# Optimization experiments

Measured on AMD Instinct MI355X. Metric: run time of the kernel, lower is better.

Reference implementation:

```python
import jax, jax.numpy as jnp
import numpy as np

N, M, H, D_IN, D_OUT = 131072, 256, 1024, 512, 512


def setup_inputs() -> dict:
    key = jax.random.key(0)
    ks = jax.random.split(key, 26)
    s = 0.05  # small init scale so gates/softplus stay in a sane range
    rn = lambda k, sh, sc=1.0: jax.random.normal(k, sh, jnp.float32) * sc
    ru = lambda k, sh: jax.random.uniform(k, sh, dtype=jnp.float32)
    pw = ru(ks[5], (2, 1, N))
    pw = pw / jnp.sum(pw, axis=-1, keepdims=True)  # prev weights are attention distributions
    return {
        'x': rn(ks[0], (1, D_IN)),
        'prev_read': rn(ks[1], (1, M)),
        'h_state': rn(ks[2], (1, H), s),
        'c_state': rn(ks[3], (1, H), s),
        'memory': ru(ks[4], (1, N, M)),
        'prev_w': pw,
        'W_ih': rn(ks[6], (4 * H, D_IN + M), s),
        'b_ih': rn(ks[7], (4 * H,), s),
        'W_hh': rn(ks[8], (4 * H, H), s),
        'b_hh': rn(ks[9], (4 * H,), s),
        'W_out': rn(ks[10], (D_OUT, H + M), s),
        'b_out': rn(ks[11], (D_OUT,), s),
        'Wk': rn(ks[12], (2, M, H), s),
        'bk': rn(ks[13], (2, M), s),
        'Wbeta': rn(ks[14], (2, H), s),
        'bbeta': rn(ks[15], (2,), s),
        'Wg': rn(ks[16], (2, H), s),
        'bg': rn(ks[17], (2,), s),
        'Ws': rn(ks[18], (2, 3, H), s),
        'bs': rn(ks[19], (2, 3), s),
        'Wgamma': rn(ks[20], (2, H), s),
        'bgamma': rn(ks[21], (2,), s),
        'We': rn(ks[22], (2, M, H), s),
        'be': rn(ks[23], (2, M), s),
        'Wa': rn(ks[24], (2, M, H), s),
        'ba': rn(ks[25], (2, M), s),
    }


def _ntm_step(x, prev_read, h_state, c_state, memory, prev_w, W_ih, b_ih, W_hh,
              b_hh, W_out, b_out, Wk, bk, Wbeta, bbeta, Wg, bg, Ws, bs,
              Wgamma, bgamma, We, be, Wa, ba):
    # ---- LSTMCell controller (torch gate order: i, f, g, o) ----
    lstm_in = jnp.concatenate([x, prev_read], axis=1)  # [1, D_IN+M]
    gates = lstm_in @ W_ih.T + b_ih + h_state @ W_hh.T + b_hh
    i_g, f_g, g_g, o_g = jnp.split(gates, 4, axis=1)
    c = jax.nn.sigmoid(f_g) * c_state + jax.nn.sigmoid(i_g) * jnp.tanh(g_g)
    h = jax.nn.sigmoid(o_g) * jnp.tanh(c)

    EPS_COS, EPS_SHARP = 1e-8, 1e-16

    def head_addr(idx, mem):
        # heads are driven by the CELL state (as in the original code)
        key_v = jnp.tanh(c @ Wk[idx].T + bk[idx])                              # [1, M]
        beta = jax.nn.softplus(jnp.sum(c * Wbeta[idx], 1, keepdims=True) + bbeta[idx])
        gate = jax.nn.sigmoid(jnp.sum(c * Wg[idx], 1, keepdims=True) + bg[idx])
        shift = jax.nn.softmax(c @ Ws[idx].T + bs[idx], axis=1)                # [1, 3]
        gamma = 1.0 + jax.nn.softplus(jnp.sum(c * Wgamma[idx], 1, keepdims=True) + bgamma[idx])
        # content addressing: cosine similarity against all N rows
        dots = jnp.einsum('bm,bnm->bn', key_v, mem)                            # [1, N]
        kn = jnp.maximum(jnp.linalg.norm(key_v, axis=1, keepdims=True), EPS_COS)
        mn = jnp.maximum(jnp.linalg.norm(mem, axis=2), EPS_COS)
        cw = jax.nn.softmax(beta * dots / (kn * mn), axis=1)
        # gated interpolation with previous weights
        gw = gate * cw + (1.0 - gate) * prev_w[idx]
        # 3-tap circular convolution shift (== conv1d on circularly padded w)
        sw = (shift[:, 0:1] * jnp.roll(gw, 1, axis=1)
              + shift[:, 1:2] * gw
              + shift[:, 2:3] * jnp.roll(gw, -1, axis=1))
        wp = sw ** gamma  # sharpening
        return wp / (jnp.sum(wp, 1, keepdims=True) + EPS_SHARP)

    # head 0: read (operates on pre-write memory)
    w_r = head_addr(0, memory)
    read = jnp.einsum('bn,bnm->bm', w_r, memory)                               # [1, M]
    # head 1: write (erase then add)
    w_w = head_addr(1, memory)
    erase = jax.nn.sigmoid(c @ We[1].T + be[1])                                # [1, M]
    add = jnp.tanh(c @ Wa[1].T + ba[1])                                        # [1, M]
    new_mem = memory * (1.0 - w_w[:, :, None] * erase[:, None, :]) \
              + w_w[:, :, None] * add[:, None, :]
    # external output
    out = jax.nn.sigmoid(jnp.concatenate([h, read], axis=1) @ W_out.T + b_out)
    return out, new_mem


def reference(x, prev_read, h_state, c_state, memory, prev_w, W_ih, b_ih, W_hh,
              b_hh, W_out, b_out, Wk, bk, Wbeta, bbeta, Wg, bg, Ws, bs,
              Wgamma, bgamma, We, be, Wa, ba):
    return _ntm_step(x, prev_read, h_state, c_state, memory, prev_w, W_ih, b_ih,
                     W_hh, b_hh, W_out, b_out, Wk, bk, Wbeta, bbeta, Wg, bg,
                     Ws, bs, Wgamma, bgamma, We, be, Wa, ba)
```

## Files before the change

### kernel.cpp

```cpp
#include <hip/hip_runtime.h>
#include <math.h>

#define NN 131072
#define MM 256
#define HH 1024

#define WS_P      0
#define WS_GATES  64
#define WS_KEY    4160
#define WS_ER     4672
#define WS_AD     4928
#define WS_E      8192
#define WS_WP     270336
#define WS_PSUM   532480
#define WS_PSUM2  548864
#define WS_RPART  549888
#define WS_READ   812032

#define P_RAWB   0
#define P_RAWG   2
#define P_RAWGA  4
#define P_RAWS   6
#define P_SSCALE 12
#define P_GATE   14
#define P_GAMMA  16
#define P_SHIFT  18
#define P_INVS   26
#define P_WSCALE 28

__device__ __forceinline__ float wave_sum(float v) {
    v += __shfl_xor(v, 32); v += __shfl_xor(v, 16); v += __shfl_xor(v, 8);
    v += __shfl_xor(v, 4);  v += __shfl_xor(v, 2);  v += __shfl_xor(v, 1);
    return v;
}
__device__ __forceinline__ float sigm(float x) { return 1.0f / (1.0f + expf(-x)); }
__device__ __forceinline__ float softplus_(float x) { return x > 20.0f ? x : log1pf(expf(x)); }
__device__ __forceinline__ float dot4(float4 a, float4 b) {
    return a.x * b.x + a.y * b.y + a.z * b.z + a.w * b.w;
}

__global__ __launch_bounds__(256) void gates_kernel(
    const float* __restrict__ x, const float* __restrict__ pr, const float* __restrict__ hs,
    const float* __restrict__ Wih, const float* __restrict__ bih,
    const float* __restrict__ Whh, const float* __restrict__ bhh,
    float* __restrict__ gates)
{
    int wid = blockIdx.x * 4 + (threadIdx.x >> 6);
    int lane = threadIdx.x & 63;
    const float4* wi4 = (const float4*)(Wih + (size_t)wid * 768);
    const float4* wh4 = (const float4*)(Whh + (size_t)wid * 1024);
    const float4* x4  = (const float4*)x;
    const float4* pr4 = (const float4*)pr;
    const float4* hs4 = (const float4*)hs;
    float s = 0.f;
    #pragma unroll
    for (int q = 0; q < 3; q++) {
        int j4 = lane + 64 * q;
        float4 wv = wi4[j4];
        float4 xv = (q < 2) ? x4[j4] : pr4[j4 - 128];
        s += dot4(wv, xv);
    }
    #pragma unroll
    for (int q = 0; q < 4; q++) {
        int j4 = lane + 64 * q;
        s += dot4(wh4[j4], hs4[j4]);
    }
    s = wave_sum(s);
    if (lane == 0) gates[wid] = s + bih[wid] + bhh[wid];
}

__global__ __launch_bounds__(256) void head_prep_kernel(
    const float* __restrict__ gates, const float* __restrict__ cs,
    const float* __restrict__ Wk, const float* __restrict__ bk,
    const float* __restrict__ We, const float* __restrict__ be,
    const float* __restrict__ Wa, const float* __restrict__ ba,
    const float* __restrict__ Ws, const float* __restrict__ bs,
    const float* __restrict__ Wbeta, const float* __restrict__ bbeta,
    const float* __restrict__ Wg, const float* __restrict__ bg,
    const float* __restrict__ Wgamma, const float* __restrict__ bgamma,
    float* __restrict__ key, float* __restrict__ er, float* __restrict__ ad,
    float* __restrict__ params)
{
    __shared__ float c_l[1024];
    int t = threadIdx.x;
    #pragma unroll
    for (int k = 0; k < 4; k++) {
        int j = t + 256 * k;
        float ig = gates[j], fg = gates[1024 + j], gg = gates[2048 + j];
        c_l[j] = sigm(fg) * cs[j] + sigm(ig) * tanhf(gg);
    }
    __syncthreads();

    int wid = blockIdx.x * 4 + (t >> 6);
    int lane = t & 63;
    const float* wrow; float bias; float* dst; int act;
    if (wid < 512)      { int h = wid >> 8, m = wid & 255; wrow = Wk + (size_t)(h * 256 + m) * 1024; bias = bk[h * 256 + m]; dst = key + wid; act = 0; }
    else if (wid < 768) { int m = wid - 512; wrow = We + (size_t)(256 + m) * 1024; bias = be[256 + m]; dst = er + m; act = 1; }
    else if (wid < 1024){ int m = wid - 768; wrow = Wa + (size_t)(256 + m) * 1024; bias = ba[256 + m]; dst = ad + m; act = 0; }
    else if (wid < 1030){ int k = wid - 1024; wrow = Ws + (size_t)k * 1024; bias = bs[k]; dst = params + P_RAWS + k; act = 2; }
    else                { int k = wid - 1030; int h = k & 1, which = k >> 1;
                          const float* Wp = which == 0 ? Wbeta : (which == 1 ? Wg : Wgamma);
                          const float* bp = which == 0 ? bbeta : (which == 1 ? bg : bgamma);
                          wrow = Wp + h * 1024; bias = bp[h]; dst = params + 2 * which + h; act = 2; }
    const float4* w4 = (const float4*)wrow;
    const float4* c4 = (const float4*)c_l;
    float s = 0.f;
    #pragma unroll
    for (int q = 0; q < 4; q++) {
        int j4 = lane + 64 * q;
        s += dot4(w4[j4], c4[j4]);
    }
    s = wave_sum(s);
    if (lane == 0) {
        s += bias;
        if (act == 0) s = tanhf(s);
        else if (act == 1) s = sigm(s);
        *dst = s;
    }
}

__global__ void finalize_params_kernel(const float* __restrict__ key, float* __restrict__ params)
{
    int h = threadIdx.x >> 6, lane = threadIdx.x & 63;
    float s = 0.f;
    for (int m = lane; m < 256; m += 64) { float v = key[h * 256 + m]; s += v * v; }
    s = wave_sum(s);
    if (lane == 0) {
        float kn = fmaxf(sqrtf(s), 1e-8f);
        params[P_SSCALE + h] = softplus_(params[P_RAWB + h]) / kn;
        params[P_GATE + h]   = sigm(params[P_RAWG + h]);
        params[P_GAMMA + h]  = 1.0f + softplus_(params[P_RAWGA + h]);
        float s0 = params[P_RAWS + h * 3], s1 = params[P_RAWS + h * 3 + 1], s2 = params[P_RAWS + h * 3 + 2];
        float mx = fmaxf(s0, fmaxf(s1, s2));
        float e0 = expf(s0 - mx), e1 = expf(s1 - mx), e2 = expf(s2 - mx);
        float inv = 1.0f / (e0 + e1 + e2);
        params[P_SHIFT + h * 3]     = e0 * inv;
        params[P_SHIFT + h * 3 + 1] = e1 * inv;
        params[P_SHIFT + h * 3 + 2] = e2 * inv;
    }
}

__global__ __launch_bounds__(256) void score_exp_kernel(
    const float* __restrict__ mem, const float* __restrict__ key,
    const float* __restrict__ params, float* __restrict__ e, float* __restrict__ psum)
{
    int w = threadIdx.x >> 6, lane = threadIdx.x & 63;
    int sub = lane & 15, g = lane >> 4;
    int wid = blockIdx.x * 4 + w;
    int row = wid * 4 + g;
    const float4* m4 = (const float4*)mem;
    const float4* k4 = (const float4*)key;
    float4 k0[4], k1[4], mv[4];
    #pragma unroll
    for (int q = 0; q < 4; q++) {
        k0[q] = k4[sub + 16 * q];
        k1[q] = k4[64 + sub + 16 * q];
        mv[q] = m4[(size_t)row * 64 + sub + 16 * q];
    }
    float d0 = 0.f, d1 = 0.f, sq = 0.f;
    #pragma unroll
    for (int q = 0; q < 4; q++) {
        d0 += dot4(k0[q], mv[q]);
        d1 += dot4(k1[q], mv[q]);
        sq += dot4(mv[q], mv[q]);
    }
    #pragma unroll
    for (int off = 8; off; off >>= 1) {
        d0 += __shfl_xor(d0, off); d1 += __shfl_xor(d1, off); sq += __shfl_xor(sq, off);
    }
    float a0 = 0.f, a1 = 0.f;
    if (sub == 0) {
        float mn = fmaxf(sqrtf(sq), 1e-8f);
        float s0 = params[P_SSCALE] * d0 / mn;
        float s1 = params[P_SSCALE + 1] * d1 / mn;
        a0 = expf(fminf(s0, 60.f));
        a1 = expf(fminf(s1, 60.f));
        e[row] = a0;
        e[NN + row] = a1;
    }
    a0 = wave_sum(a0); a1 = wave_sum(a1);
    __shared__ float l[8];
    if (lane == 0) { l[w] = a0; l[4 + w] = a1; }
    __syncthreads();
    if (threadIdx.x == 0) {
        psum[blockIdx.x]        = l[0] + l[1] + l[2] + l[3];
        psum[8192 + blockIdx.x] = l[4] + l[5] + l[6] + l[7];
    }
}

__global__ void reduce_inv_kernel(const float* __restrict__ psum, float* __restrict__ dst,
                                  int n, float eps)
{
    float v0 = 0.f, v1 = 0.f;
    for (int i = threadIdx.x; i < n; i += 1024) { v0 += psum[i]; v1 += psum[n + i]; }
    v0 = wave_sum(v0); v1 = wave_sum(v1);
    __shared__ float l[32];
    int w = threadIdx.x >> 6, lane = threadIdx.x & 63;
    if (lane == 0) { l[w] = v0; l[16 + w] = v1; }
    __syncthreads();
    if (threadIdx.x == 0) {
        float S0 = 0.f, S1 = 0.f;
        for (int i = 0; i < 16; i++) { S0 += l[i]; S1 += l[16 + i]; }
        dst[0] = 1.0f / (S0 + eps);
        dst[1] = 1.0f / (S1 + eps);
    }
}

__global__ __launch_bounds__(256) void shift_pow_kernel(
    const float* __restrict__ e, const float* __restrict__ pw,
    const float* __restrict__ params, float* __restrict__ wp, float* __restrict__ psum2)
{
    int tid = blockIdx.x * 256 + threadIdx.x;
    float gate0 = params[P_GATE], gate1 = params[P_GATE + 1];
    float inv0 = params[P_INVS], inv1 = params[P_INVS + 1];
    float ga0 = params[P_GAMMA], ga1 = params[P_GAMMA + 1];
    float sh00 = params[P_SHIFT], sh01 = params[P_SHIFT + 1], sh02 = params[P_SHIFT + 2];
    float sh10 = params[P_SHIFT + 3], sh11 = params[P_SHIFT + 4], sh12 = params[P_SHIFT + 5];
    float a0 = 0.f, a1 = 0.f;
    for (int h = 0; h < 2; h++) {
        int n = tid;
        int base = h << 17;
        float gate = h ? gate1 : gate0, inv = h ? inv1 : inv0, gamma = h ? ga1 : ga0;
        float s0 = h ? sh10 : sh00, s1 = h ? sh11 : sh01, s2 = h ? sh12 : sh02;
        int nm = (n - 1) & (NN - 1), np = (n + 1) & (NN - 1);
        float gwm = gate * e[base + nm] * inv + (1.f - gate) * pw[base + nm];
        float gw0 = gate * e[base + n] * inv + (1.f - gate) * pw[base + n];
        float gwp = gate * e[base + np] * inv + (1.f - gate) * pw[base + np];
        float sw = s0 * gwm + s1 * gw0 + s2 * gwp;
        float v = powf(sw, gamma);
        wp[base + n] = v;
        if (h) a1 += v; else a0 += v;
    }
    a0 = wave_sum(a0); a1 = wave_sum(a1);
    __shared__ float l[8];
    int w = threadIdx.x >> 6, lane = threadIdx.x & 63;
    if (lane == 0) { l[w] = a0; l[4 + w] = a1; }
    __syncthreads();
    if (threadIdx.x == 0) {
        psum2[blockIdx.x]       = l[0] + l[1] + l[2] + l[3];
        psum2[512 + blockIdx.x] = l[4] + l[5] + l[6] + l[7];
    }
}

__global__ __launch_bounds__(256) void update_kernel(
    const float* __restrict__ mem, const float* __restrict__ wp,
    const float* __restrict__ params, const float* __restrict__ er, const float* __restrict__ ad,
    float* __restrict__ newmem, float* __restrict__ rpart)
{
    int w = threadIdx.x >> 6, lane = threadIdx.x & 63;
    int wid = blockIdx.x * 4 + w;
    float sc0 = params[P_WSCALE], sc1 = params[P_WSCALE + 1];
    float4 e4 = ((const float4*)er)[lane];
    float4 a4 = ((const float4*)ad)[lane];
    float4 acc = make_float4(0.f, 0.f, 0.f, 0.f);
    const float4* m4 = (const float4*)mem;
    float4* o4 = (float4*)newmem;
    for (int r = 0; r < 32; r++) {
        int row = wid * 32 + r;
        float wr = wp[row] * sc0;
        float ww = wp[NN + row] * sc1;
        float4 mv = m4[(size_t)row * 64 + lane];
        float4 nm;
        nm.x = mv.x * (1.f - ww * e4.x) + ww * a4.x;
        nm.y = mv.y * (1.f - ww * e4.y) + ww * a4.y;
        nm.z = mv.z * (1.f - ww * e4.z) + ww * a4.z;
        nm.w = mv.w * (1.f - ww * e4.w) + ww * a4.w;
        o4[(size_t)row * 64 + lane] = nm;
        acc.x += wr * mv.x; acc.y += wr * mv.y; acc.z += wr * mv.z; acc.w += wr * mv.w;
    }
    __shared__ float lds[4][256];
    lds[w][lane * 4 + 0] = acc.x;
    lds[w][lane * 4 + 1] = acc.y;
    lds[w][lane * 4 + 2] = acc.z;
    lds[w][lane * 4 + 3] = acc.w;
    __syncthreads();
    int tid = threadIdx.x;
    float s = lds[0][tid] + lds[1][tid] + lds[2][tid] + lds[3][tid];
    rpart[(size_t)blockIdx.x * 256 + tid] = s;
}

__global__ __launch_bounds__(256) void read_reduce_kernel(
    const float* __restrict__ rpart, float* __restrict__ readv)
{
    int m = blockIdx.x;
    int t = threadIdx.x;
    float s = 0.f;
    #pragma unroll
    for (int k = 0; k < 4; k++) s += rpart[(size_t)(t + 256 * k) * 256 + m];
    s = wave_sum(s);
    __shared__ float l[4];
    int w = t >> 6, lane = t & 63;
    if (lane == 0) l[w] = s;
    __syncthreads();
    if (t == 0) readv[m] = l[0] + l[1] + l[2] + l[3];
}

__global__ __launch_bounds__(256) void out_kernel(
    const float* __restrict__ gates, const float* __restrict__ cs,
    const float* __restrict__ readv,
    const float* __restrict__ Wout, const float* __restrict__ bout, float* __restrict__ out)
{
    __shared__ float hl[1280];
    int t = threadIdx.x;
    #pragma unroll
    for (int k = 0; k < 4; k++) {
        int j = t + 256 * k;
        float ig = gates[j], fg = gates[1024 + j], gg = gates[2048 + j], og = gates[3072 + j];
        float cv = sigm(fg) * cs[j] + sigm(ig) * tanhf(gg);
        hl[j] = sigm(og) * tanhf(cv);
    }
    hl[1024 + t] = readv[t];
    __syncthreads();

    int wid = blockIdx.x * 4 + (t >> 6);
    int lane = t & 63;
    const float4* w4 = (const float4*)(Wout + (size_t)wid * 1280);
    const float4* h4 = (const float4*)hl;
    float s = 0.f;
    #pragma unroll
    for (int q = 0; q < 5; q++) {
        int j4 = lane + 64 * q;
        s += dot4(w4[j4], h4[j4]);
    }
    s = wave_sum(s);
    if (lane == 0) out[wid] = sigm(s + bout[wid]);
}

extern "C" void kernel_launch(void* const* d_in, const int* in_sizes, int n_in,
                              void* d_out, int out_size, void* d_ws, size_t ws_size,
                              hipStream_t stream)
{
    const float* x       = (const float*)d_in[0];
    const float* pr      = (const float*)d_in[1];
    const float* hs      = (const float*)d_in[2];
    const float* cs      = (const float*)d_in[3];
    const float* mem     = (const float*)d_in[4];
    const float* pw      = (const float*)d_in[5];
    const float* Wih     = (const float*)d_in[6];
    const float* bih     = (const float*)d_in[7];
    const float* Whh     = (const float*)d_in[8];
    const float* bhh     = (const float*)d_in[9];
    const float* Wout    = (const float*)d_in[10];
    const float* bout    = (const float*)d_in[11];
    const float* Wk      = (const float*)d_in[12];
    const float* bk      = (const float*)d_in[13];
    const float* Wbeta   = (const float*)d_in[14];
    const float* bbeta   = (const float*)d_in[15];
    const float* Wg      = (const float*)d_in[16];
    const float* bg      = (const float*)d_in[17];
    const float* Ws      = (const float*)d_in[18];
    const float* bs      = (const float*)d_in[19];
    const float* Wgamma  = (const float*)d_in[20];
    const float* bgamma  = (const float*)d_in[21];
    const float* We      = (const float*)d_in[22];
    const float* be      = (const float*)d_in[23];
    const float* Wa      = (const float*)d_in[24];
    const float* ba      = (const float*)d_in[25];

    float* ws = (float*)d_ws;
    float* P      = ws + WS_P;
    float* gates  = ws + WS_GATES;
    float* key    = ws + WS_KEY;
    float* er     = ws + WS_ER;
    float* ad     = ws + WS_AD;
    float* e      = ws + WS_E;
    float* wp     = ws + WS_WP;
    float* psum   = ws + WS_PSUM;
    float* psum2  = ws + WS_PSUM2;
    float* rpart  = ws + WS_RPART;
    float* readv  = ws + WS_READ;

    float* out    = (float*)d_out;
    float* newmem = (float*)d_out + 512;

    gates_kernel<<<1024, 256, 0, stream>>>(x, pr, hs, Wih, bih, Whh, bhh, gates);
    head_prep_kernel<<<259, 256, 0, stream>>>(gates, cs, Wk, bk, We, be, Wa, ba, Ws, bs,
                                              Wbeta, bbeta, Wg, bg, Wgamma, bgamma,
                                              key, er, ad, P);
    finalize_params_kernel<<<1, 128, 0, stream>>>(key, P);
    score_exp_kernel<<<8192, 256, 0, stream>>>(mem, key, P, e, psum);
    reduce_inv_kernel<<<1, 1024, 0, stream>>>(psum, P + P_INVS, 8192, 0.0f);
    shift_pow_kernel<<<512, 256, 0, stream>>>(e, pw, P, wp, psum2);
    reduce_inv_kernel<<<1, 1024, 0, stream>>>(psum2, P + P_WSCALE, 512, 1e-16f);
    update_kernel<<<1024, 256, 0, stream>>>(mem, wp, P, er, ad, newmem, rpart);
    read_reduce_kernel<<<256, 256, 0, stream>>>(rpart, readv);
    out_kernel<<<128, 256, 0, stream>>>(gates, cs, readv, Wout, bout, out);
}
```

Before: 109.3 us.

## Fold scalar param and reduction kernels into consumer kernel prologues

Removes the finalize_params kernel and both single-block reduce_inv launches. Each consumer block now recomputes the key norm, the 8192-entry partial-sum reduction or the 512-entry reduction redundantly in its own prologue. This cuts three serialized launches and their gaps, at the cost of redundant per-block reads and extra barriers. It also switches exp and pow to the fast intrinsics and makes the new-memory writes nontemporal stores.

```diff
diff --git a/kernel.cpp b/kernel.cpp
--- a/kernel.cpp
+++ b/kernel.cpp
@@ -4,6 +4,8 @@
 #define NN 131072
 #define MM 256
 #define HH 1024
+
+typedef float nat_f4 __attribute__((ext_vector_type(4)));
 
 #define WS_P      0
 #define WS_GATES  64
@@ -21,12 +23,6 @@
 #define P_RAWG   2
 #define P_RAWGA  4
 #define P_RAWS   6
-#define P_SSCALE 12
-#define P_GATE   14
-#define P_GAMMA  16
-#define P_SHIFT  18
-#define P_INVS   26
-#define P_WSCALE 28
 
 __device__ __forceinline__ float wave_sum(float v) {
     v += __shfl_xor(v, 32); v += __shfl_xor(v, 16); v += __shfl_xor(v, 8);
@@ -119,32 +115,28 @@
     }
 }
 
-__global__ void finalize_params_kernel(const float* __restrict__ key, float* __restrict__ params)
-{
-    int h = threadIdx.x >> 6, lane = threadIdx.x & 63;
-    float s = 0.f;
-    for (int m = lane; m < 256; m += 64) { float v = key[h * 256 + m]; s += v * v; }
-    s = wave_sum(s);
-    if (lane == 0) {
-        float kn = fmaxf(sqrtf(s), 1e-8f);
-        params[P_SSCALE + h] = softplus_(params[P_RAWB + h]) / kn;
-        params[P_GATE + h]   = sigm(params[P_RAWG + h]);
-        params[P_GAMMA + h]  = 1.0f + softplus_(params[P_RAWGA + h]);
-        float s0 = params[P_RAWS + h * 3], s1 = params[P_RAWS + h * 3 + 1], s2 = params[P_RAWS + h * 3 + 2];
-        float mx = fmaxf(s0, fmaxf(s1, s2));
-        float e0 = expf(s0 - mx), e1 = expf(s1 - mx), e2 = expf(s2 - mx);
-        float inv = 1.0f / (e0 + e1 + e2);
-        params[P_SHIFT + h * 3]     = e0 * inv;
-        params[P_SHIFT + h * 3 + 1] = e1 * inv;
-        params[P_SHIFT + h * 3 + 2] = e2 * inv;
-    }
-}
-
 __global__ __launch_bounds__(256) void score_exp_kernel(
     const float* __restrict__ mem, const float* __restrict__ key,
     const float* __restrict__ params, float* __restrict__ e, float* __restrict__ psum)
 {
-    int w = threadIdx.x >> 6, lane = threadIdx.x & 63;
+    __shared__ float ss_l[2];
+    __shared__ float red[8];
+    int t = threadIdx.x;
+    int w = t >> 6, lane = t & 63;
+    {
+        float v0 = key[t], v1 = key[256 + t];
+        float s0 = v0 * v0, s1 = v1 * v1;
+        s0 = wave_sum(s0); s1 = wave_sum(s1);
+        if (lane == 0) { red[w] = s0; red[4 + w] = s1; }
+        __syncthreads();
+        if (t == 0) {
+            float k0 = red[0] + red[1] + red[2] + red[3];
+            float k1 = red[4] + red[5] + red[6] + red[7];
+            ss_l[0] = softplus_(params[P_RAWB])     / fmaxf(sqrtf(k0), 1e-8f);
+            ss_l[1] = softplus_(params[P_RAWB + 1]) / fmaxf(sqrtf(k1), 1e-8f);
+        }
+        __syncthreads();
+    }
     int sub = lane & 15, g = lane >> 4;
     int wid = blockIdx.x * 4 + w;
     int row = wid * 4 + g;
@@ -171,52 +163,69 @@
     float a0 = 0.f, a1 = 0.f;
     if (sub == 0) {
         float mn = fmaxf(sqrtf(sq), 1e-8f);
-        float s0 = params[P_SSCALE] * d0 / mn;
-        float s1 = params[P_SSCALE + 1] * d1 / mn;
-        a0 = expf(fminf(s0, 60.f));
-        a1 = expf(fminf(s1, 60.f));
+        float s0 = ss_l[0] * d0 / mn;
+        float s1 = ss_l[1] * d1 / mn;
+        a0 = __expf(fminf(s0, 60.f));
+        a1 = __expf(fminf(s1, 60.f));
         e[row] = a0;
         e[NN + row] = a1;
     }
     a0 = wave_sum(a0); a1 = wave_sum(a1);
-    __shared__ float l[8];
-    if (lane == 0) { l[w] = a0; l[4 + w] = a1; }
-    __syncthreads();
-    if (threadIdx.x == 0) {
-        psum[blockIdx.x]        = l[0] + l[1] + l[2] + l[3];
-        psum[8192 + blockIdx.x] = l[4] + l[5] + l[6] + l[7];
-    }
-}
-
-__global__ void reduce_inv_kernel(const float* __restrict__ psum, float* __restrict__ dst,
-                                  int n, float eps)
-{
-    float v0 = 0.f, v1 = 0.f;
-    for (int i = threadIdx.x; i < n; i += 1024) { v0 += psum[i]; v1 += psum[n + i]; }
-    v0 = wave_sum(v0); v1 = wave_sum(v1);
-    __shared__ float l[32];
-    int w = threadIdx.x >> 6, lane = threadIdx.x & 63;
-    if (lane == 0) { l[w] = v0; l[16 + w] = v1; }
-    __syncthreads();
-    if (threadIdx.x == 0) {
-        float S0 = 0.f, S1 = 0.f;
-        for (int i = 0; i < 16; i++) { S0 += l[i]; S1 += l[16 + i]; }
-        dst[0] = 1.0f / (S0 + eps);
-        dst[1] = 1.0f / (S1 + eps);
+    __syncthreads();
+    if (lane == 0) { red[w] = a0; red[4 + w] = a1; }
+    __syncthreads();
+    if (t == 0) {
+        psum[blockIdx.x]        = red[0] + red[1] + red[2] + red[3];
+        psum[8192 + blockIdx.x] = red[4] + red[5] + red[6] + red[7];
     }
 }
 
 __global__ __launch_bounds__(256) void shift_pow_kernel(
     const float* __restrict__ e, const float* __restrict__ pw,
-    const float* __restrict__ params, float* __restrict__ wp, float* __restrict__ psum2)
-{
-    int tid = blockIdx.x * 256 + threadIdx.x;
-    float gate0 = params[P_GATE], gate1 = params[P_GATE + 1];
-    float inv0 = params[P_INVS], inv1 = params[P_INVS + 1];
-    float ga0 = params[P_GAMMA], ga1 = params[P_GAMMA + 1];
-    float sh00 = params[P_SHIFT], sh01 = params[P_SHIFT + 1], sh02 = params[P_SHIFT + 2];
-    float sh10 = params[P_SHIFT + 3], sh11 = params[P_SHIFT + 4], sh12 = params[P_SHIFT + 5];
+    const float* __restrict__ params, const float* __restrict__ psum,
+    float* __restrict__ wp, float* __restrict__ psum2)
+{
+    __shared__ float par[6];
+    __shared__ float shs[6];
+    __shared__ float red[8];
+    int t = threadIdx.x;
+    int w = t >> 6, lane = t & 63;
+    {
+        float v0 = 0.f, v1 = 0.f;
+        for (int i = t; i < 8192; i += 256) { v0 += psum[i]; v1 += psum[8192 + i]; }
+        v0 = wave_sum(v0); v1 = wave_sum(v1);
+        if (lane == 0) { red[w] = v0; red[4 + w] = v1; }
+        __syncthreads();
+        if (t == 0) {
+            par[0] = 1.0f / (red[0] + red[1] + red[2] + red[3]);
+            par[1] = 1.0f / (red[4] + red[5] + red[6] + red[7]);
+            par[2] = sigm(params[P_RAWG]);
+            par[3] = sigm(params[P_RAWG + 1]);
+            par[4] = 1.0f + softplus_(params[P_RAWGA]);
+            par[5] = 1.0f + softplus_(params[P_RAWGA + 1]);
+        }
+        if (t == 64) {
+            #pragma unroll
+            for (int h = 0; h < 2; h++) {
+                float s0 = params[P_RAWS + h * 3], s1 = params[P_RAWS + h * 3 + 1], s2 = params[P_RAWS + h * 3 + 2];
+                float mx = fmaxf(s0, fmaxf(s1, s2));
+                float e0 = expf(s0 - mx), e1 = expf(s1 - mx), e2 = expf(s2 - mx);
+                float inv = 1.0f / (e0 + e1 + e2);
+                shs[h * 3 + 0] = e0 * inv;
+                shs[h * 3 + 1] = e1 * inv;
+                shs[h * 3 + 2] = e2 * inv;
+            }
+        }
+        __syncthreads();
+    }
+    float gate0 = par[2], gate1 = par[3];
+    float inv0 = par[0], inv1 = par[1];
+    float ga0 = par[4], ga1 = par[5];
+    float sh00 = shs[0], sh01 = shs[1], sh02 = shs[2];
+    float sh10 = shs[3], sh11 = shs[4], sh12 = shs[5];
+    int tid = blockIdx.x * 256 + t;
     float a0 = 0.f, a1 = 0.f;
+    #pragma unroll
     for (int h = 0; h < 2; h++) {
         int n = tid;
         int base = h << 17;
@@ -227,45 +236,59 @@
         float gw0 = gate * e[base + n] * inv + (1.f - gate) * pw[base + n];
         float gwp = gate * e[base + np] * inv + (1.f - gate) * pw[base + np];
         float sw = s0 * gwm + s1 * gw0 + s2 * gwp;
-        float v = powf(sw, gamma);
+        float v = __powf(sw, gamma);
         wp[base + n] = v;
         if (h) a1 += v; else a0 += v;
     }
     a0 = wave_sum(a0); a1 = wave_sum(a1);
-    __shared__ float l[8];
-    int w = threadIdx.x >> 6, lane = threadIdx.x & 63;
-    if (lane == 0) { l[w] = a0; l[4 + w] = a1; }
-    __syncthreads();
-    if (threadIdx.x == 0) {
-        psum2[blockIdx.x]       = l[0] + l[1] + l[2] + l[3];
-        psum2[512 + blockIdx.x] = l[4] + l[5] + l[6] + l[7];
+    __syncthreads();
+    if (lane == 0) { red[w] = a0; red[4 + w] = a1; }
+    __syncthreads();
+    if (t == 0) {
+        psum2[blockIdx.x]       = red[0] + red[1] + red[2] + red[3];
+        psum2[512 + blockIdx.x] = red[4] + red[5] + red[6] + red[7];
     }
 }
 
 __global__ __launch_bounds__(256) void update_kernel(
     const float* __restrict__ mem, const float* __restrict__ wp,
-    const float* __restrict__ params, const float* __restrict__ er, const float* __restrict__ ad,
+    const float* __restrict__ psum2, const float* __restrict__ er, const float* __restrict__ ad,
     float* __restrict__ newmem, float* __restrict__ rpart)
 {
-    int w = threadIdx.x >> 6, lane = threadIdx.x & 63;
+    __shared__ float sc_l[2];
+    __shared__ float red[8];
+    int t = threadIdx.x;
+    int w = t >> 6, lane = t & 63;
+    {
+        float v0 = 0.f, v1 = 0.f;
+        for (int i = t; i < 512; i += 256) { v0 += psum2[i]; v1 += psum2[512 + i]; }
+        v0 = wave_sum(v0); v1 = wave_sum(v1);
+        if (lane == 0) { red[w] = v0; red[4 + w] = v1; }
+        __syncthreads();
+        if (t == 0) {
+            sc_l[0] = 1.0f / (red[0] + red[1] + red[2] + red[3] + 1e-16f);
+            sc_l[1] = 1.0f / (red[4] + red[5] + red[6] + red[7] + 1e-16f);
+        }
+        __syncthreads();
+    }
+    float sc0 = sc_l[0], sc1 = sc_l[1];
     int wid = blockIdx.x * 4 + w;
-    float sc0 = params[P_WSCALE], sc1 = params[P_WSCALE + 1];
     float4 e4 = ((const float4*)er)[lane];
     float4 a4 = ((const float4*)ad)[lane];
     float4 acc = make_float4(0.f, 0.f, 0.f, 0.f);
     const float4* m4 = (const float4*)mem;
-    float4* o4 = (float4*)newmem;
+    nat_f4* o4 = (nat_f4*)newmem;
     for (int r = 0; r < 32; r++) {
         int row = wid * 32 + r;
         float wr = wp[row] * sc0;
         float ww = wp[NN + row] * sc1;
         float4 mv = m4[(size_t)row * 64 + lane];
-        float4 nm;
+        nat_f4 nm;
         nm.x = mv.x * (1.f - ww * e4.x) + ww * a4.x;
         nm.y = mv.y * (1.f - ww * e4.y) + ww * a4.y;
         nm.z = mv.z * (1.f - ww * e4.z) + ww * a4.z;
         nm.w = mv.w * (1.f - ww * e4.w) + ww * a4.w;
-        o4[(size_t)row * 64 + lane] = nm;
+        __builtin_nontemporal_store(nm, &o4[(size_t)row * 64 + lane]);
         acc.x += wr * mv.x; acc.y += wr * mv.y; acc.z += wr * mv.z; acc.w += wr * mv.w;
     }
     __shared__ float lds[4][256];
@@ -274,9 +297,8 @@
     lds[w][lane * 4 + 2] = acc.z;
     lds[w][lane * 4 + 3] = acc.w;
     __syncthreads();
-    int tid = threadIdx.x;
-    float s = lds[0][tid] + lds[1][tid] + lds[2][tid] + lds[3][tid];
-    rpart[(size_t)blockIdx.x * 256 + tid] = s;
+    float s = lds[0][t] + lds[1][t] + lds[2][t] + lds[3][t];
+    rpart[(size_t)blockIdx.x * 256 + t] = s;
 }
 
 __global__ __launch_bounds__(256) void read_reduce_kernel(
@@ -377,12 +399,9 @@
     head_prep_kernel<<<259, 256, 0, stream>>>(gates, cs, Wk, bk, We, be, Wa, ba, Ws, bs,
                                               Wbeta, bbeta, Wg, bg, Wgamma, bgamma,
                                               key, er, ad, P);
-    finalize_params_kernel<<<1, 128, 0, stream>>>(key, P);
     score_exp_kernel<<<8192, 256, 0, stream>>>(mem, key, P, e, psum);
-    reduce_inv_kernel<<<1, 1024, 0, stream>>>(psum, P + P_INVS, 8192, 0.0f);
-    shift_pow_kernel<<<512, 256, 0, stream>>>(e, pw, P, wp, psum2);
-    reduce_inv_kernel<<<1, 1024, 0, stream>>>(psum2, P + P_WSCALE, 512, 1e-16f);
-    update_kernel<<<1024, 256, 0, stream>>>(mem, wp, P, er, ad, newmem, rpart);
+    shift_pow_kernel<<<512, 256, 0, stream>>>(e, pw, P, psum, wp, psum2);
+    update_kernel<<<1024, 256, 0, stream>>>(mem, wp, psum2, er, ad, newmem, rpart);
     read_reduce_kernel<<<256, 256, 0, stream>>>(rpart, readv);
     out_kernel<<<128, 256, 0, stream>>>(gates, cs, readv, Wout, bout, out);
 }
```

Result: faster. 106.7 us (median of 2 runs) (-2.4%).
